# Kernel tuning notes

Hardware: AMD Instinct MI355X
Metric: run time of the kernel (lower is better)

Reference implementation:

```python
import jax, jax.numpy as jnp
import numpy as np

L = 6      # layers (enc and dec)
D = 512    # d_model
H = 8      # heads
DK = D // H
F = 2048   # dim_feedforward
B = 8
S = 512    # src len
T = 512    # tgt len
NEG = -1e9


def setup_inputs() -> dict:
    key = jax.random.key(0)
    ks = jax.random.split(key, 64)
    it = iter(ks)
    def w(shape, scale=0.02):
        return jax.random.normal(next(it), shape, dtype=jnp.float32) * scale
    inp = {}
    inp['src'] = jax.random.normal(next(it), (B, S, D), dtype=jnp.float32)
    inp['tgt'] = jax.random.normal(next(it), (B, T, D), dtype=jnp.float32)
    inp['tgt_mask'] = jnp.where(jnp.triu(jnp.ones((T, T), bool), 1), jnp.float32(NEG), jnp.float32(0.0))
    # encoder params (stacked over L layers)
    inp['enc_Wq'] = w((L, H, D, DK)); inp['enc_Wk'] = w((L, H, D, DK)); inp['enc_Wv'] = w((L, H, D, DK))
    inp['enc_Wo'] = w((L, D, D))
    inp['enc_ln1_a'] = jnp.ones((L, D)); inp['enc_ln1_b'] = jnp.zeros((L, D))
    inp['enc_W1'] = w((L, D, F)); inp['enc_b1'] = jnp.zeros((L, F))
    inp['enc_W2'] = w((L, F, D)); inp['enc_b2'] = jnp.zeros((L, D))
    inp['enc_ln2_a'] = jnp.ones((L, D)); inp['enc_ln2_b'] = jnp.zeros((L, D))
    # decoder params
    inp['dec_sWq'] = w((L, H, D, DK)); inp['dec_sWk'] = w((L, H, D, DK)); inp['dec_sWv'] = w((L, H, D, DK))
    inp['dec_sWo'] = w((L, D, D))
    inp['dec_ln1_a'] = jnp.ones((L, D)); inp['dec_ln1_b'] = jnp.zeros((L, D))
    inp['dec_cWq'] = w((L, H, D, DK)); inp['dec_cWk'] = w((L, H, D, DK)); inp['dec_cWv'] = w((L, H, D, DK))
    inp['dec_cWo'] = w((L, D, D))
    inp['dec_ln2_a'] = jnp.ones((L, D)); inp['dec_ln2_b'] = jnp.zeros((L, D))
    inp['dec_W1'] = w((L, D, F)); inp['dec_b1'] = jnp.zeros((L, F))
    inp['dec_W2'] = w((L, F, D)); inp['dec_b2'] = jnp.zeros((L, D))
    inp['dec_ln3_a'] = jnp.ones((L, D)); inp['dec_ln3_b'] = jnp.zeros((L, D))
    return inp


def layernorm(x, a, b):
    # faithful to the torch module: unbiased std (ddof=1) and eps added to std
    mean = x.mean(-1, keepdims=True)
    std = jnp.std(x, axis=-1, keepdims=True, ddof=1)
    return a * (x - mean) / (std + 1e-6) + b


def mha(qx, kx, vx, Wq, Wk, Wv, Wo, mask):
    # Wq/Wk/Wv: [H, D, dk] (per-head torch loop fused into one batched einsum)
    q = jnp.einsum('bsd,hdk->bhsk', qx, Wq)
    k = jnp.einsum('bsd,hdk->bhsk', kx, Wk)
    v = jnp.einsum('bsd,hdk->bhsk', vx, Wv)
    scores = jnp.einsum('bhqk,bhmk->bhqm', q, k) / np.float32(np.sqrt(Wq.shape[-1]))
    if mask is not None:
        scores = scores + mask  # [T,T] broadcasts over batch and heads
    attn = jax.nn.softmax(scores, axis=-1)
    o = jnp.einsum('bhqm,bhmk->bhqk', attn, v)
    b_, h_, s_, k_ = o.shape
    o = o.transpose(0, 2, 1, 3).reshape(b_, s_, h_ * k_)  # concat heads
    return o @ Wo


def ffn(x, W1, b1, W2, b2):
    return jnp.maximum(x @ W1 + b1, 0.0) @ W2 + b2


def reference(src, tgt, tgt_mask,
              enc_Wq, enc_Wk, enc_Wv, enc_Wo, enc_ln1_a, enc_ln1_b,
              enc_W1, enc_b1, enc_W2, enc_b2, enc_ln2_a, enc_ln2_b,
              dec_sWq, dec_sWk, dec_sWv, dec_sWo, dec_ln1_a, dec_ln1_b,
              dec_cWq, dec_cWk, dec_cWv, dec_cWo, dec_ln2_a, dec_ln2_b,
              dec_W1, dec_b1, dec_W2, dec_b2, dec_ln3_a, dec_ln3_b):
    # encoder
    x = src
    for i in range(L):
        h = x + mha(x, x, x, enc_Wq[i], enc_Wk[i], enc_Wv[i], enc_Wo[i], None)
        x = layernorm(h, enc_ln1_a[i], enc_ln1_b[i])
        h = x + ffn(x, enc_W1[i], enc_b1[i], enc_W2[i], enc_b2[i])
        x = layernorm(h, enc_ln2_a[i], enc_ln2_b[i])
    memory = x
    # decoder
    y = tgt
    for i in range(L):
        h = y + mha(y, y, y, dec_sWq[i], dec_sWk[i], dec_sWv[i], dec_sWo[i], tgt_mask)
        y = layernorm(h, dec_ln1_a[i], dec_ln1_b[i])
        h = y + mha(y, memory, memory, dec_cWq[i], dec_cWk[i], dec_cWv[i], dec_cWo[i], None)
        y = layernorm(h, dec_ln2_a[i], dec_ln2_b[i])
        h = y + ffn(y, dec_W1[i], dec_b1[i], dec_W2[i], dec_b2[i])
        y = layernorm(h, dec_ln3_a[i], dec_ln3_b[i])
    return y
```

## Files before the change

### kernel.cpp

```cpp
#include <hip/hip_runtime.h>
#include <hip/hip_bf16.h>

typedef unsigned short u16;
typedef __hip_bfloat16 hbf;
typedef __bf16 bf16x8 __attribute__((ext_vector_type(8)));
typedef float f32x4 __attribute__((ext_vector_type(4)));

#define LL 6
#define DD 512
#define HH 8
#define DKK 64
#define FF 2048
#define BB 8
#define SS 512

__global__ __launch_bounds__(256) void cvt_k(const float* __restrict__ x,
                                             hbf* __restrict__ y, int n) {
  for (int i = (blockIdx.x * 256 + threadIdx.x) * 4; i < n; i += gridDim.x * 1024) {
    float4 v = *(const float4*)(x + i);
    y[i] = __float2bfloat16(v.x);
    y[i + 1] = __float2bfloat16(v.y);
    y[i + 2] = __float2bfloat16(v.z);
    y[i + 3] = __float2bfloat16(v.w);
  }
}

__global__ __launch_bounds__(256) void transpose_k(const float* __restrict__ src,
                                                   hbf* __restrict__ dst, int R, int C) {
  __shared__ hbf tile[64][65];
  const int b = blockIdx.z;
  src += (size_t)b * R * C;
  dst += (size_t)b * R * C;
  int c0 = blockIdx.x * 64, r0 = blockIdx.y * 64;
  int tx = threadIdx.x & 63;
  int ty = threadIdx.x >> 6;
#pragma unroll
  for (int i = 0; i < 16; i++) {
    int r = ty + i * 4;
    tile[r][tx] = __float2bfloat16(src[(size_t)(r0 + r) * C + c0 + tx]);
  }
  __syncthreads();
#pragma unroll
  for (int i = 0; i < 16; i++) {
    int r = ty + i * 4;
    dst[(size_t)(c0 + r) * R + r0 + tx] = tile[tx][r];
  }
}

__global__ __launch_bounds__(256) void transpose_qkv_k(const float* __restrict__ Wq,
                                                       const float* __restrict__ Wk,
                                                       const float* __restrict__ Wv,
                                                       hbf* __restrict__ dst) {
  __shared__ hbf tile[64][65];
  const int z = blockIdx.z;
  const int l = z / 24, r = z - l * 24;
  const int zw = r >> 3, h = r & 7;
  const float* src =
      (zw == 0 ? Wq : (zw == 1 ? Wk : Wv)) + ((size_t)l * HH + h) * DD * DKK;
  const int r0 = blockIdx.y * 64;
  const int tx = threadIdx.x & 63, ty = threadIdx.x >> 6;
#pragma unroll
  for (int i = 0; i < 16; i++) {
    int rr = ty + i * 4;
    tile[rr][tx] = __float2bfloat16(src[(size_t)(r0 + rr) * DKK + tx]);
  }
  __syncthreads();
  hbf* d = dst + (size_t)l * 3 * DD * DD + ((size_t)zw * 512 + h * 64) * DD + r0;
#pragma unroll
  for (int i = 0; i < 16; i++) {
    int rr = ty + i * 4;
    d[(size_t)rr * DD + tx] = tile[tx][rr];
  }
}

template <int BM, int BN, int BK, int MODE, int SPLITK>
__global__ __launch_bounds__(256) void gemm_nt(
    const u16* __restrict__ A, const u16* __restrict__ Bm, void* __restrict__ Cout,
    void* __restrict__ C2, void* __restrict__ C3,
    const float* __restrict__ bias, const hbf* __restrict__ res,
    int M, int N, int K, int lda, int ldb, int ldc, int ncoloff,
    long sAo, long sAi, long sBo, long sBi, long sCo, long sCi, int inner, float scale) {
  constexpr int WVM = (BM == 128 && BN == 128) ? 2 : (BM == 128 ? 4 : 2);
  constexpr int WVN = 4 / WVM;
  constexpr int WTM = BM / WVM, WTN = BN / WVN;
  constexpr int AM = WTM / 16, AN = WTN / 16;
  constexpr int PA = (BM * BK) / 2048, PB = (BN * BK) / 2048;
  constexpr int CPR = BK / 8;
  __shared__ u16 As[BM][BK + 8];
  __shared__ u16 Bs[BN][BK + 8];

  int g = blockIdx.z;
  int ks = 0;
  if (SPLITK > 1) {
    ks = g;
    g = 0;
  }
  int outer = g / inner, inr = g - outer * inner;
  A += outer * sAo + inr * sAi;
  Bm += outer * sBo + inr * sBi;

  const int tid = threadIdx.x;
  const int m0 = blockIdx.y * BM, n0 = (blockIdx.x + ncoloff) * BN;
  const int wave = tid >> 6, lane = tid & 63;
  const int wm = (wave / WVN) * WTM, wn = (wave % WVN) * WTN;
  const int m16 = lane & 15, quad = lane >> 4;

  const u16* Ab = A + (size_t)m0 * lda;
  const u16* Bb = Bm + (size_t)n0 * ldb;

  f32x4 acc[AM][AN] = {};

  const int kbeg = ks * (K / SPLITK), kend = kbeg + K / SPLITK;
  for (int k0 = kbeg; k0 < kend; k0 += BK) {
#pragma unroll
    for (int p = 0; p < PA; p++) {
      int idx = p * 256 + tid;
      int row = idx / CPR, ch = (idx % CPR) * 8;
      *(float4*)(&As[row][ch]) = *(const float4*)(Ab + (size_t)row * lda + k0 + ch);
    }
#pragma unroll
    for (int p = 0; p < PB; p++) {
      int idx = p * 256 + tid;
      int row = idx / CPR, ch = (idx % CPR) * 8;
      *(float4*)(&Bs[row][ch]) = *(const float4*)(Bb + (size_t)row * ldb + k0 + ch);
    }
    __syncthreads();
#pragma unroll
    for (int kc = 0; kc < BK / 32; kc++) {
      bf16x8 af[AM], bfv[AN];
#pragma unroll
      for (int i = 0; i < AM; i++)
        af[i] = *(const bf16x8*)(&As[wm + i * 16 + m16][kc * 32 + quad * 8]);
#pragma unroll
      for (int j = 0; j < AN; j++)
        bfv[j] = *(const bf16x8*)(&Bs[wn + j * 16 + m16][kc * 32 + quad * 8]);
#pragma unroll
      for (int i = 0; i < AM; i++)
#pragma unroll
        for (int j = 0; j < AN; j++)
          acc[i][j] = __builtin_amdgcn_mfma_f32_16x16x32_bf16(af[i], bfv[j], acc[i][j], 0, 0, 0);
    }
    __syncthreads();
  }

#pragma unroll
  for (int i = 0; i < AM; i++) {
#pragma unroll
    for (int j = 0; j < AN; j++) {
      const int col = n0 + wn + j * 16 + m16;
      const int rowb = m0 + wm + i * 16 + quad * 4;
#pragma unroll
      for (int r = 0; r < 4; r++) {
        const int row = rowb + r;
        float v = acc[i][j][r] * scale;
        if (MODE == 0) {
          hbf* C = (hbf*)Cout + outer * sCo + inr * sCi;
          C[(size_t)row * ldc + col] = __float2bfloat16(v);
        } else if (MODE == 2) {
          float* C = (float*)((SPLITK > 1 && ks == 1) ? C2 : Cout);
          C += outer * sCo + inr * sCi;
          if (SPLITK == 1 || ks == 0) {
            if (bias) v += bias[col];
            if (res) v += __bfloat162float(res[(size_t)row * ldc + col]);
          }
          C[(size_t)row * ldc + col] = v;
        } else if (MODE == 3) {
          hbf* C = (hbf*)Cout + outer * sCo + inr * sCi;
          v += bias[col];
          C[(size_t)row * ldc + col] = __float2bfloat16(fmaxf(v, 0.0f));
        } else if (MODE == 4) {
          const int b = row >> 9, s = row & 511;
          const int which = col >> 9, h = (col >> 6) & 7, dk = col & 63;
          const int bh = (b << 3) + h;
          if (which == 0)
            ((hbf*)Cout)[((size_t)bh * SS + s) * DKK + dk] = __float2bfloat16(v * 0.125f);
          else if (which == 1)
            ((hbf*)C2)[((size_t)bh * SS + s) * DKK + dk] = __float2bfloat16(v);
          else
            ((hbf*)C3)[((size_t)bh * DKK + dk) * SS + s] = __float2bfloat16(v);
        }
      }
    }
  }
}

__global__ __launch_bounds__(256) void flash_k(const u16* __restrict__ Q,
                                               const u16* __restrict__ Kb,
                                               const u16* __restrict__ Vt,
                                               hbf* __restrict__ O, int causal) {
  __shared__ u16 Qs[32][72];
  __shared__ u16 Ks[128 * 72];
  __shared__ u16 Ss[32][520];
  const int bh = blockIdx.y;
  const int q0 = blockIdx.x * 32;
  const int b = bh >> 3, h = bh & 7;
  const int tid = threadIdx.x;
  const int wave = tid >> 6, lane = tid & 63;
  const int m16 = lane & 15, quad = lane >> 4;
  const int rg = (wave >> 1) * 16;
  const int chf = wave & 1;

  const u16* Qp = Q + ((size_t)bh * SS + q0) * DKK;
  const u16* Kp = Kb + (size_t)bh * SS * DKK;
  const u16* Vp = Vt + (size_t)bh * DKK * SS;

  {
    int row = tid >> 3, ch = (tid & 7) << 3;
    *(float4*)(&Qs[row][ch]) = *(const float4*)(Qp + (size_t)row * DKK + ch);
  }

  for (int kt = 0; kt < 4; kt++) {
    if (kt > 0) __syncthreads();
#pragma unroll
    for (int p = 0; p < 4; p++) {
      int idx = p * 256 + tid;
      int row = idx >> 3, ch = (idx & 7) << 3;
      *(float4*)(&Ks[row * 72 + ch]) =
          *(const float4*)(Kp + (size_t)(kt * 128 + row) * DKK + ch);
    }
    __syncthreads();
#pragma unroll
    for (int ct = 0; ct < 4; ct++) {
      f32x4 s{};
#pragma unroll
      for (int kc = 0; kc < 2; kc++) {
        bf16x8 a = *(const bf16x8*)(&Qs[rg + m16][kc * 32 + quad * 8]);
        bf16x8 bv =
            *(const bf16x8*)(&Ks[(chf * 64 + ct * 16 + m16) * 72 + kc * 32 + quad * 8]);
        s = __builtin_amdgcn_mfma_f32_16x16x32_bf16(a, bv, s, 0, 0, 0);
      }
      const int colb = kt * 128 + chf * 64 + ct * 16 + m16;
#pragma unroll
      for (int r = 0; r < 4; r++)
        *((hbf*)&Ss[rg + quad * 4 + r][colb]) = __float2bfloat16(s[r]);
    }
  }
  __syncthreads();

#pragma unroll
  for (int rr = 0; rr < 8; rr++) {
    const int r = wave * 8 + rr;
    const int gr = q0 + r;
    float v[8];
#pragma unroll
    for (int i = 0; i < 8; i++) {
      const int col = lane + i * 64;
      v[i] = __bfloat162float(((const hbf*)Ss[r])[col]);
      if (causal && col > gr) v[i] = -1e30f;
    }
    float m = v[0];
#pragma unroll
    for (int i = 1; i < 8; i++) m = fmaxf(m, v[i]);
#pragma unroll
    for (int off = 1; off < 64; off <<= 1) m = fmaxf(m, __shfl_xor(m, off));
    float e[8], s = 0.f;
#pragma unroll
    for (int i = 0; i < 8; i++) {
      e[i] = __expf(v[i] - m);
      s += e[i];
    }
#pragma unroll
    for (int off = 1; off < 64; off <<= 1) s += __shfl_xor(s, off);
    const float inv = 1.0f / s;
#pragma unroll
    for (int i = 0; i < 8; i++)
      ((hbf*)Ss[r])[lane + i * 64] = __float2bfloat16(e[i] * inv);
  }
  __syncthreads();

  f32x4 o[2] = {};
  u16* Vs = Ks;
  for (int vt = 0; vt < 4; vt++) {
    if (vt > 0) __syncthreads();
#pragma unroll
    for (int p = 0; p < 4; p++) {
      int idx = p * 256 + tid;
      int row = idx >> 4, ch = (idx & 15) << 3;
      *(float4*)(&Vs[row * 136 + ch]) =
          *(const float4*)(Vp + (size_t)row * SS + vt * 128 + ch);
    }
    __syncthreads();
#pragma unroll
    for (int kc = 0; kc < 4; kc++) {
      bf16x8 a = *(const bf16x8*)(&Ss[rg + m16][vt * 128 + kc * 32 + quad * 8]);
#pragma unroll
      for (int dt = 0; dt < 2; dt++) {
        bf16x8 bv =
            *(const bf16x8*)(&Vs[(chf * 32 + dt * 16 + m16) * 136 + kc * 32 + quad * 8]);
        o[dt] = __builtin_amdgcn_mfma_f32_16x16x32_bf16(a, bv, o[dt], 0, 0, 0);
      }
    }
  }
#pragma unroll
  for (int dt = 0; dt < 2; dt++) {
    const int d = h * 64 + chf * 32 + dt * 16 + m16;
#pragma unroll
    for (int r = 0; r < 4; r++) {
      const int row = q0 + rg + quad * 4 + r;
      O[(size_t)b * SS * DD + (size_t)row * DD + d] = __float2bfloat16(o[dt][r]);
    }
  }
}

template <typename T>
__global__ __launch_bounds__(256) void layernorm_k(const float* __restrict__ X,
                                                   const float* __restrict__ X2,
                                                   const float* __restrict__ ga,
                                                   const float* __restrict__ gb,
                                                   T* __restrict__ out, int Dn) {
  const int row = blockIdx.x;
  X += (size_t)row * Dn;
  X2 += (size_t)row * Dn;
  out += (size_t)row * Dn;
  const int t = threadIdx.x;
  float2 xv = *(const float2*)(X + 2 * t);
  float2 x2 = *(const float2*)(X2 + 2 * t);
  xv.x += x2.x;
  xv.y += x2.y;
  float s = xv.x + xv.y, ss = xv.x * xv.x + xv.y * xv.y;
#pragma unroll
  for (int off = 32; off > 0; off >>= 1) {
    s += __shfl_down(s, off);
    ss += __shfl_down(ss, off);
  }
  __shared__ float sm[8];
  __shared__ float smean, sinv;
  const int wv = t >> 6, ln = t & 63;
  if (ln == 0) {
    sm[wv] = s;
    sm[4 + wv] = ss;
  }
  __syncthreads();
  if (t == 0) {
    float S1 = sm[0] + sm[1] + sm[2] + sm[3];
    float S2 = sm[4] + sm[5] + sm[6] + sm[7];
    float mean = S1 / Dn;
    float var = (S2 - S1 * mean) / (Dn - 1);
    var = fmaxf(var, 0.0f);
    smean = mean;
    sinv = 1.0f / (sqrtf(var) + 1e-6f);
  }
  __syncthreads();
  const float mean = smean, inv = sinv;
  float o0 = ga[2 * t] * (xv.x - mean) * inv + gb[2 * t];
  float o1 = ga[2 * t + 1] * (xv.y - mean) * inv + gb[2 * t + 1];
  if constexpr (sizeof(T) == 2) {
    out[2 * t] = (T)__float2bfloat16(o0);
    out[2 * t + 1] = (T)__float2bfloat16(o1);
  } else {
    out[2 * t] = o0;
    out[2 * t + 1] = o1;
  }
}

extern "C" void kernel_launch(void* const* d_in, const int* in_sizes, int n_in,
                              void* d_out, int out_size, void* d_ws, size_t ws_size,
                              hipStream_t stream) {
  (void)in_sizes; (void)n_in; (void)out_size;
  const float* src = (const float*)d_in[0];
  const float* tgt = (const float*)d_in[1];
  const float* eWq = (const float*)d_in[3];
  const float* eWk = (const float*)d_in[4];
  const float* eWv = (const float*)d_in[5];
  const float* eWo = (const float*)d_in[6];
  const float* eln1a = (const float*)d_in[7];
  const float* eln1b = (const float*)d_in[8];
  const float* eW1 = (const float*)d_in[9];
  const float* eb1 = (const float*)d_in[10];
  const float* eW2 = (const float*)d_in[11];
  const float* eb2 = (const float*)d_in[12];
  const float* eln2a = (const float*)d_in[13];
  const float* eln2b = (const float*)d_in[14];
  const float* sWq = (const float*)d_in[15];
  const float* sWk = (const float*)d_in[16];
  const float* sWv = (const float*)d_in[17];
  const float* sWo = (const float*)d_in[18];
  const float* dln1a = (const float*)d_in[19];
  const float* dln1b = (const float*)d_in[20];
  const float* cWq = (const float*)d_in[21];
  const float* cWk = (const float*)d_in[22];
  const float* cWv = (const float*)d_in[23];
  const float* cWo = (const float*)d_in[24];
  const float* dln2a = (const float*)d_in[25];
  const float* dln2b = (const float*)d_in[26];
  const float* dW1 = (const float*)d_in[27];
  const float* db1 = (const float*)d_in[28];
  const float* dW2 = (const float*)d_in[29];
  const float* db2 = (const float*)d_in[30];
  const float* dln3a = (const float*)d_in[31];
  const float* dln3b = (const float*)d_in[32];

  const size_t MB = 1024 * 1024;
  char* ws = (char*)d_ws;
  const size_t QKV_L = (size_t)3 * DD * DD;
  const size_t WO_L = (size_t)DD * DD;
  const size_t WF_L = (size_t)DD * FF;
  const bool preT = ws_size >= 150 * MB;

  hbf *qkvT_all = nullptr, *woT_all = nullptr, *w1T_all = nullptr, *w2T_all = nullptr;
  hbf *wqkvS = nullptr, *woS = nullptr, *w1S = nullptr, *w2S = nullptr;
  char* actb;
  if (preT) {
    qkvT_all = (hbf*)(ws);
    woT_all = (hbf*)(ws + 28311552);
    w1T_all = (hbf*)(ws + 37748736);
    w2T_all = (hbf*)(ws + 62914560);
    actb = ws + 84 * MB;
  } else {
    if (ws_size < 72 * MB) return;
    wqkvS = (hbf*)(ws);
    woS = (hbf*)(ws + 2 * MB);
    w1S = (hbf*)(ws + 2 * MB + 512 * 1024);
    w2S = (hbf*)(ws + 4 * MB + 512 * 1024);
    actb = ws + 7 * MB;
  }
  hbf* sbuf = (hbf*)(actb);
  u16* xbuf = (u16*)(actb + 4 * MB);
  hbf* tbuf = (hbf*)(actb + 8 * MB);
  u16* ybuf = (u16*)(actb + 12 * MB);
  u16* qbuf = (u16*)(actb + 16 * MB);
  u16* kbuf = (u16*)(actb + 20 * MB);
  u16* vtb = (u16*)(actb + 24 * MB);
  u16* obuf = (u16*)(actb + 28 * MB);
  u16* ffnh = (u16*)(actb + 32 * MB);
  float* projf = (float*)(actb + 48 * MB);
  float* projf2 = (float*)(actb + 56 * MB);

  const size_t WQL = (size_t)HH * DD * DKK;
  const size_t WOL = (size_t)DD * DD;
  const size_t WFL = (size_t)DD * FF;

  if (preT) {
    transpose_qkv_k<<<dim3(1, 8, LL * 24), dim3(256), 0, stream>>>(eWq, eWk, eWv, qkvT_all);
    transpose_qkv_k<<<dim3(1, 8, LL * 24), dim3(256), 0, stream>>>(sWq, sWk, sWv,
                                                                   qkvT_all + LL * QKV_L);
    transpose_qkv_k<<<dim3(1, 8, LL * 24), dim3(256), 0, stream>>>(
        cWq, cWk, cWv, qkvT_all + 2 * LL * QKV_L);
    transpose_k<<<dim3(8, 8, LL), dim3(256), 0, stream>>>(eWo, woT_all, DD, DD);
    transpose_k<<<dim3(8, 8, LL), dim3(256), 0, stream>>>(sWo, woT_all + LL * WO_L, DD, DD);
    transpose_k<<<dim3(8, 8, LL), dim3(256), 0, stream>>>(cWo, woT_all + 2 * LL * WO_L, DD, DD);
    transpose_k<<<dim3(32, 8, LL), dim3(256), 0, stream>>>(eW1, w1T_all, DD, FF);
    transpose_k<<<dim3(32, 8, LL), dim3(256), 0, stream>>>(dW1, w1T_all + LL * WF_L, DD, FF);
    transpose_k<<<dim3(8, 32, LL), dim3(256), 0, stream>>>(eW2, w2T_all, FF, DD);
    transpose_k<<<dim3(8, 32, LL), dim3(256), 0, stream>>>(dW2, w2T_all + LL * WF_L, FF, DD);
  }

  auto attention = [&](const u16* qin, const u16* kvin, const hbf* qkvTl, const hbf* woTl,
                       const u16* resid, int causal) {
    if (qin == kvin) {
      gemm_nt<64, 64, 128, 4, 1><<<dim3(24, 64, 1), dim3(256), 0, stream>>>(
          qin, (const u16*)qkvTl, qbuf, kbuf, vtb, nullptr, nullptr, BB * SS, 3 * DD, DD,
          DD, DD, 0, 0, 0, 0, 0, 0, 0, 0, 1, 1.f);
    } else {
      gemm_nt<64, 64, 128, 4, 1><<<dim3(8, 64, 1), dim3(256), 0, stream>>>(
          qin, (const u16*)qkvTl, qbuf, kbuf, vtb, nullptr, nullptr, BB * SS, DD, DD,
          DD, DD, 0, 0, 0, 0, 0, 0, 0, 0, 1, 1.f);
      gemm_nt<64, 64, 128, 4, 1><<<dim3(16, 64, 1), dim3(256), 0, stream>>>(
          kvin, (const u16*)qkvTl, qbuf, kbuf, vtb, nullptr, nullptr, BB * SS, 3 * DD, DD,
          DD, DD, 0, 8, 0, 0, 0, 0, 0, 0, 1, 1.f);
    }
    flash_k<<<dim3(16, 64), dim3(256), 0, stream>>>(qbuf, kbuf, vtb, (hbf*)obuf, causal);
    gemm_nt<64, 64, 128, 2, 2><<<dim3(8, 64, 2), dim3(256), 0, stream>>>(
        obuf, (const u16*)woTl, projf, projf2, nullptr, nullptr, (const hbf*)resid,
        BB * SS, DD, DD, DD, DD, DD, 0, 0, 0, 0, 0, 0, 0, 1, 1.f);
  };

  auto ffn = [&](const u16* xin, const hbf* w1Tl, const float* b1l, const hbf* w2Tl,
                 const float* b2l) {
    gemm_nt<64, 64, 128, 3, 1><<<dim3(32, 64, 1), dim3(256), 0, stream>>>(
        xin, (const u16*)w1Tl, ffnh, nullptr, nullptr, b1l, nullptr, BB * SS, FF, DD,
        DD, DD, FF, 0, 0, 0, 0, 0, 0, 0, 1, 1.f);
    gemm_nt<64, 64, 128, 2, 2><<<dim3(8, 64, 2), dim3(256), 0, stream>>>(
        ffnh, (const u16*)w2Tl, projf, projf2, nullptr, b2l, (const hbf*)xin, BB * SS, DD,
        FF, FF, FF, DD, 0, 0, 0, 0, 0, 0, 0, 1, 1.f);
  };

  auto lnb = [&](const float* X, const float* a, const float* b, u16* out) {
    layernorm_k<hbf><<<dim3(BB * SS), dim3(256), 0, stream>>>(X, projf2, a, b, (hbf*)out, DD);
  };

  cvt_k<<<dim3(2048), dim3(256), 0, stream>>>(src, sbuf, BB * SS * DD);
  cvt_k<<<dim3(2048), dim3(256), 0, stream>>>(tgt, tbuf, BB * SS * DD);

  const u16* cur = (const u16*)sbuf;
  for (int l = 0; l < LL; l++) {
    const hbf *qkvTl, *woTl, *w1Tl, *w2Tl;
    if (preT) {
      qkvTl = qkvT_all + (size_t)l * QKV_L;
      woTl = woT_all + (size_t)l * WO_L;
      w1Tl = w1T_all + (size_t)l * WF_L;
      w2Tl = w2T_all + (size_t)l * WF_L;
    } else {
      transpose_qkv_k<<<dim3(1, 8, 24), dim3(256), 0, stream>>>(
          eWq + l * WQL, eWk + l * WQL, eWv + l * WQL, wqkvS);
      transpose_k<<<dim3(8, 8, 1), dim3(256), 0, stream>>>(eWo + l * WOL, woS, DD, DD);
      qkvTl = wqkvS;
      woTl = woS;
    }
    attention(cur, cur, qkvTl, woTl, cur, 0);
    lnb(projf, eln1a + l * DD, eln1b + l * DD, xbuf);
    if (!preT) {
      transpose_k<<<dim3(32, 8, 1), dim3(256), 0, stream>>>(eW1 + l * WFL, w1S, DD, FF);
      transpose_k<<<dim3(8, 32, 1), dim3(256), 0, stream>>>(eW2 + l * WFL, w2S, FF, DD);
      w1Tl = w1S;
      w2Tl = w2S;
    }
    ffn(xbuf, w1Tl, eb1 + l * FF, w2Tl, eb2 + l * DD);
    lnb(projf, eln2a + l * DD, eln2b + l * DD, xbuf);
    cur = xbuf;
  }
  const u16* mem = cur;
  const u16* yc = (const u16*)tbuf;
  for (int l = 0; l < LL; l++) {
    const hbf *sqkvTl, *swoTl, *cqkvTl, *cwoTl, *w1Tl, *w2Tl;
    if (preT) {
      sqkvTl = qkvT_all + ((size_t)LL + l) * QKV_L;
      swoTl = woT_all + ((size_t)LL + l) * WO_L;
      cqkvTl = qkvT_all + ((size_t)2 * LL + l) * QKV_L;
      cwoTl = woT_all + ((size_t)2 * LL + l) * WO_L;
      w1Tl = w1T_all + ((size_t)LL + l) * WF_L;
      w2Tl = w2T_all + ((size_t)LL + l) * WF_L;
    }
    if (!preT) {
      transpose_qkv_k<<<dim3(1, 8, 24), dim3(256), 0, stream>>>(
          sWq + l * WQL, sWk + l * WQL, sWv + l * WQL, wqkvS);
      transpose_k<<<dim3(8, 8, 1), dim3(256), 0, stream>>>(sWo + l * WOL, woS, DD, DD);
      sqkvTl = wqkvS;
      swoTl = woS;
    }
    attention(yc, yc, sqkvTl, swoTl, yc, 1);
    lnb(projf, dln1a + l * DD, dln1b + l * DD, ybuf);
    yc = ybuf;
    if (!preT) {
      transpose_qkv_k<<<dim3(1, 8, 24), dim3(256), 0, stream>>>(
          cWq + l * WQL, cWk + l * WQL, cWv + l * WQL, wqkvS);
      transpose_k<<<dim3(8, 8, 1), dim3(256), 0, stream>>>(cWo + l * WOL, woS, DD, DD);
      cqkvTl = wqkvS;
      cwoTl = woS;
    }
    attention(yc, mem, cqkvTl, cwoTl, yc, 0);
    lnb(projf, dln2a + l * DD, dln2b + l * DD, ybuf);
    if (!preT) {
      transpose_k<<<dim3(32, 8, 1), dim3(256), 0, stream>>>(dW1 + l * WFL, w1S, DD, FF);
      transpose_k<<<dim3(8, 32, 1), dim3(256), 0, stream>>>(dW2 + l * WFL, w2S, FF, DD);
      w1Tl = w1S;
      w2Tl = w2S;
    }
    ffn(ybuf, w1Tl, db1 + l * FF, w2Tl, db2 + l * DD);
    if (l == LL - 1) {
      layernorm_k<float><<<dim3(BB * SS), dim3(256), 0, stream>>>(
          projf, projf2, dln3a + l * DD, dln3b + l * DD, (float*)d_out, DD);
    } else {
      lnb(projf, dln3a + l * DD, dln3b + l * DD, ybuf);
      yc = ybuf;
    }
  }
}
```

Measured before the change: 2.171 ms.

## Use 128x128 GEMM tiles with direct global-to-LDS loads and XOR swizzle

The GEMM kernel is rewritten to a fixed 128x128x64 tile with four waves, each computing a 64x64 sub-tile. Shared-memory staging now uses global_load_lds, so loads go straight to LDS without passing through registers. An XOR swizzle on the column chunk replaces the padded layout to avoid bank conflicts. Larger tiles raise data reuse and MFMA density, but they halve the grid sizes, which may reduce occupancy on smaller GEMMs such as the Wo projection (128 blocks with split-K).

Result: slower. 2.568 ms (+18.3%).

```diff
diff --git a/kernel.cpp b/kernel.cpp
--- a/kernel.cpp
+++ b/kernel.cpp
@@ -13,6 +13,11 @@
 #define FF 2048
 #define BB 8
 #define SS 512
+
+#define GLL(gp, lp)                                                        \
+  __builtin_amdgcn_global_load_lds(                                        \
+      (const __attribute__((address_space(1))) void*)(gp),                 \
+      (__attribute__((address_space(3))) void*)(lp), 16, 0, 0)
 
 __global__ __launch_bounds__(256) void cvt_k(const float* __restrict__ x,
                                              hbf* __restrict__ y, int n) {
@@ -73,21 +78,16 @@
   }
 }
 
-template <int BM, int BN, int BK, int MODE, int SPLITK>
+template <int MODE, int SPLITK>
 __global__ __launch_bounds__(256) void gemm_nt(
     const u16* __restrict__ A, const u16* __restrict__ Bm, void* __restrict__ Cout,
     void* __restrict__ C2, void* __restrict__ C3,
     const float* __restrict__ bias, const hbf* __restrict__ res,
     int M, int N, int K, int lda, int ldb, int ldc, int ncoloff,
     long sAo, long sAi, long sBo, long sBi, long sCo, long sCi, int inner, float scale) {
-  constexpr int WVM = (BM == 128 && BN == 128) ? 2 : (BM == 128 ? 4 : 2);
-  constexpr int WVN = 4 / WVM;
-  constexpr int WTM = BM / WVM, WTN = BN / WVN;
-  constexpr int AM = WTM / 16, AN = WTN / 16;
-  constexpr int PA = (BM * BK) / 2048, PB = (BN * BK) / 2048;
-  constexpr int CPR = BK / 8;
-  __shared__ u16 As[BM][BK + 8];
-  __shared__ u16 Bs[BN][BK + 8];
+  constexpr int BM = 128, BN = 128, BK = 64;
+  __shared__ u16 As[BM * BK];
+  __shared__ u16 Bs[BN * BK];
 
   int g = blockIdx.z;
   int ks = 0;
@@ -102,51 +102,53 @@
   const int tid = threadIdx.x;
   const int m0 = blockIdx.y * BM, n0 = (blockIdx.x + ncoloff) * BN;
   const int wave = tid >> 6, lane = tid & 63;
-  const int wm = (wave / WVN) * WTM, wn = (wave % WVN) * WTN;
+  const int wm = (wave >> 1) * 64, wn = (wave & 1) * 64;
   const int m16 = lane & 15, quad = lane >> 4;
-
-  const u16* Ab = A + (size_t)m0 * lda;
-  const u16* Bb = Bm + (size_t)n0 * ldb;
-
-  f32x4 acc[AM][AN] = {};
+  const int ln8 = lane & 7, ld8 = lane >> 3;
+  const int scol = (ln8 ^ ld8) << 3;
+
+  const u16* Ab = A + (size_t)m0 * lda + scol;
+  const u16* Bb = Bm + (size_t)n0 * ldb + scol;
+
+  f32x4 acc[4][4] = {};
 
   const int kbeg = ks * (K / SPLITK), kend = kbeg + K / SPLITK;
   for (int k0 = kbeg; k0 < kend; k0 += BK) {
 #pragma unroll
-    for (int p = 0; p < PA; p++) {
-      int idx = p * 256 + tid;
-      int row = idx / CPR, ch = (idx % CPR) * 8;
-      *(float4*)(&As[row][ch]) = *(const float4*)(Ab + (size_t)row * lda + k0 + ch);
-    }
-#pragma unroll
-    for (int p = 0; p < PB; p++) {
-      int idx = p * 256 + tid;
-      int row = idx / CPR, ch = (idx % CPR) * 8;
-      *(float4*)(&Bs[row][ch]) = *(const float4*)(Bb + (size_t)row * ldb + k0 + ch);
+    for (int c = 0; c < 4; c++) {
+      const int chunk = wave * 4 + c;
+      const int row = chunk * 8 + ld8;
+      GLL(Ab + (size_t)row * lda + k0, &As[chunk * 512]);
+      GLL(Bb + (size_t)row * ldb + k0, &Bs[chunk * 512]);
     }
     __syncthreads();
 #pragma unroll
-    for (int kc = 0; kc < BK / 32; kc++) {
-      bf16x8 af[AM], bfv[AN];
-#pragma unroll
-      for (int i = 0; i < AM; i++)
-        af[i] = *(const bf16x8*)(&As[wm + i * 16 + m16][kc * 32 + quad * 8]);
-#pragma unroll
-      for (int j = 0; j < AN; j++)
-        bfv[j] = *(const bf16x8*)(&Bs[wn + j * 16 + m16][kc * 32 + quad * 8]);
-#pragma unroll
-      for (int i = 0; i < AM; i++)
-#pragma unroll
-        for (int j = 0; j < AN; j++)
+    for (int kc = 0; kc < 2; kc++) {
+      bf16x8 af[4], bfv[4];
+      const int kq = (kc << 2) | quad;
+#pragma unroll
+      for (int i = 0; i < 4; i++) {
+        const int r = wm + i * 16 + m16;
+        af[i] = *(const bf16x8*)(&As[r * 64 + ((kq ^ (m16 & 7)) << 3)]);
+      }
+#pragma unroll
+      for (int j = 0; j < 4; j++) {
+        const int r = wn + j * 16 + m16;
+        bfv[j] = *(const bf16x8*)(&Bs[r * 64 + ((kq ^ (m16 & 7)) << 3)]);
+      }
+#pragma unroll
+      for (int i = 0; i < 4; i++)
+#pragma unroll
+        for (int j = 0; j < 4; j++)
           acc[i][j] = __builtin_amdgcn_mfma_f32_16x16x32_bf16(af[i], bfv[j], acc[i][j], 0, 0, 0);
     }
     __syncthreads();
   }
 
 #pragma unroll
-  for (int i = 0; i < AM; i++) {
-#pragma unroll
-    for (int j = 0; j < AN; j++) {
+  for (int i = 0; i < 4; i++) {
+#pragma unroll
+    for (int j = 0; j < 4; j++) {
       const int col = n0 + wn + j * 16 + m16;
       const int rowb = m0 + wm + i * 16 + quad * 4;
 #pragma unroll
@@ -448,29 +450,29 @@
   auto attention = [&](const u16* qin, const u16* kvin, const hbf* qkvTl, const hbf* woTl,
                        const u16* resid, int causal) {
     if (qin == kvin) {
-      gemm_nt<64, 64, 128, 4, 1><<<dim3(24, 64, 1), dim3(256), 0, stream>>>(
+      gemm_nt<4, 1><<<dim3(12, 32, 1), dim3(256), 0, stream>>>(
           qin, (const u16*)qkvTl, qbuf, kbuf, vtb, nullptr, nullptr, BB * SS, 3 * DD, DD,
           DD, DD, 0, 0, 0, 0, 0, 0, 0, 0, 1, 1.f);
     } else {
-      gemm_nt<64, 64, 128, 4, 1><<<dim3(8, 64, 1), dim3(256), 0, stream>>>(
+      gemm_nt<4, 1><<<dim3(4, 32, 1), dim3(256), 0, stream>>>(
           qin, (const u16*)qkvTl, qbuf, kbuf, vtb, nullptr, nullptr, BB * SS, DD, DD,
           DD, DD, 0, 0, 0, 0, 0, 0, 0, 0, 1, 1.f);
-      gemm_nt<64, 64, 128, 4, 1><<<dim3(16, 64, 1), dim3(256), 0, stream>>>(
+      gemm_nt<4, 1><<<dim3(8, 32, 1), dim3(256), 0, stream>>>(
           kvin, (const u16*)qkvTl, qbuf, kbuf, vtb, nullptr, nullptr, BB * SS, 3 * DD, DD,
-          DD, DD, 0, 8, 0, 0, 0, 0, 0, 0, 1, 1.f);
+          DD, DD, 0, 4, 0, 0, 0, 0, 0, 0, 1, 1.f);
     }
     flash_k<<<dim3(16, 64), dim3(256), 0, stream>>>(qbuf, kbuf, vtb, (hbf*)obuf, causal);
-    gemm_nt<64, 64, 128, 2, 2><<<dim3(8, 64, 2), dim3(256), 0, stream>>>(
+    gemm_nt<2, 2><<<dim3(4, 32, 2), dim3(256), 0, stream>>>(
         obuf, (const u16*)woTl, projf, projf2, nullptr, nullptr, (const hbf*)resid,
         BB * SS, DD, DD, DD, DD, DD, 0, 0, 0, 0, 0, 0, 0, 1, 1.f);
   };
 
   auto ffn = [&](const u16* xin, const hbf* w1Tl, const float* b1l, const hbf* w2Tl,
                  const float* b2l) {
-    gemm_nt<64, 64, 128, 3, 1><<<dim3(32, 64, 1), dim3(256), 0, stream>>>(
+    gemm_nt<3, 1><<<dim3(16, 32, 1), dim3(256), 0, stream>>>(
         xin, (const u16*)w1Tl, ffnh, nullptr, nullptr, b1l, nullptr, BB * SS, FF, DD,
         DD, DD, FF, 0, 0, 0, 0, 0, 0, 0, 1, 1.f);
-    gemm_nt<64, 64, 128, 2, 2><<<dim3(8, 64, 2), dim3(256), 0, stream>>>(
+    gemm_nt<2, 2><<<dim3(4, 32, 2), dim3(256), 0, stream>>>(
         ffnh, (const u16*)w2Tl, projf, projf2, nullptr, b2l, (const hbf*)xin, BB * SS, DD,
         FF, FF, FF, DD, 0, 0, 0, 0, 0, 0, 0, 1, 1.f);
   };
```
